# Kernel optimization log

Measured on AMD Instinct MI355X. Metric: run time of the kernel, lower is better.

Reference implementation:

```python
import jax, jax.numpy as jnp
import numpy as np

B, L, C, S, D = 2, 64, 256, 256, 512

def setup_inputs() -> dict:
    key = jax.random.key(0)
    ks = jax.random.split(key, 6)
    scale = 1.0 / np.sqrt(D)
    return {
        "queries": jax.random.normal(ks[0], (B, L, C, D), dtype=jnp.float32),
        "keys": jax.random.normal(ks[1], (B, L, S, D), dtype=jnp.float32),
        "values": jax.random.normal(ks[2], (B, L, S, D), dtype=jnp.float32),
        "Wq": jax.random.normal(ks[3], (D, D), dtype=jnp.float32) * scale,
        "bq": jnp.zeros((D,), dtype=jnp.float32),
        "Wkv": jax.random.normal(ks[4], (D, D), dtype=jnp.float32) * scale,
        "bkv": jnp.zeros((D,), dtype=jnp.float32),
        "Wo": jax.random.normal(ks[5], (D, D), dtype=jnp.float32) * scale,
        "bo": jnp.zeros((D,), dtype=jnp.float32),
    }

def reference(queries, keys, values, Wq, bq, Wkv, bkv, Wo, bo):
    d = queries.shape[-1]
    scale = 1.0 / jnp.sqrt(jnp.asarray(d, queries.dtype))
    # linear projections (torch Linear: x @ W.T + b); kv_projection shared for K and V
    q = queries @ Wq.T + bq            # [B, L, C, D]
    k = keys @ Wkv.T + bkv             # [B, L, S, D]
    v = values @ Wkv.T + bkv           # [B, L, S, D]
    scores = jnp.einsum('blcd,blsd->blcs', q, k)
    attn = jax.nn.softmax(scale * scores, axis=-1)  # dropout is identity in eval
    out = jnp.einsum('blcs,blsd->blcd', attn, v)
    return out @ Wo.T + bo
```

## Files before the change

kernel.cpp:

```cpp
#include <hip/hip_runtime.h>
#include <hip/hip_fp16.h>
#include <stdint.h>


typedef _Float16 f16;
typedef __attribute__((ext_vector_type(8))) _Float16 f16x8;
typedef __attribute__((ext_vector_type(4))) _Float16 f16x4;
typedef __attribute__((ext_vector_type(4))) float f32x4;

#define BK 64

__device__ __forceinline__ void glds16(const void* g, void* l)
{
    __builtin_amdgcn_global_load_lds(
        (const __attribute__((address_space(1))) void*)(uintptr_t)g,
        (__attribute__((address_space(3))) void*)(uint32_t)(uintptr_t)l,
        16, 0, 0);
}

__global__ __launch_bounds__(256)
void proj3(const float* __restrict__ qin, const float* __restrict__ kin,
           const float* __restrict__ vin, const f16* __restrict__ wq,
           const f16* __restrict__ wkv, const float* __restrict__ bq,
           const float* __restrict__ bkv, f16* __restrict__ qh,
           f16* __restrict__ kh, f16* __restrict__ vT)
{
    __shared__ __align__(16) float Asf[128][64];
    __shared__ __align__(16) f16  Bs[128][64];

    const int p     = blockIdx.x;
    const int which = p >> 10;
    const int inner = p & 1023;
    const int xcd   = inner & 7;
    const int slot  = inner >> 3;
    const int m0 = (xcd + 8 * (slot >> 2)) * 128;
    const int n0 = (slot & 3) * 128;

    const float* A    = (which == 0) ? qin : (which == 1) ? kin : vin;
    const f16*   Bt   = (which == 0) ? wq : wkv;
    const float* bias = (which == 0) ? bq : bkv;

    const int tid  = threadIdx.x;
    const int lane = tid & 63;
    const int wave = tid >> 6;
    const int quad = lane >> 4;
    const int l16  = lane & 15;
    const int wr   = wave >> 1;
    const int wc   = wave & 1;

    f32x4 acc[4][4];
    #pragma unroll
    for (int i = 0; i < 4; ++i)
        #pragma unroll
        for (int j = 0; j < 4; ++j)
            acc[i][j] = (f32x4){0.f, 0.f, 0.f, 0.f};

    const int i8 = lane >> 3;
    const int cl = (((lane & 7) - i8) & 7) * 8;

    const int ar4 = lane >> 4;

    for (int k0 = 0; k0 < 512; k0 += BK) {
        if (k0) __syncthreads();
        #pragma unroll
        for (int g = 0; g < 8; ++g) {
            const int R0  = (wave * 8 + g) * 4;
            const int row = R0 + ar4;
            const int gcol = ((lane & 15) - (row & 7)) & 15;
            glds16(A + (long)(m0 + row) * 512 + k0 + gcol * 4, &Asf[R0][0]);
        }
        #pragma unroll
        for (int g = 0; g < 4; ++g) {
            const int R0 = (wave * 4 + g) * 8;
            glds16(Bt + (long)(n0 + R0 + i8) * 512 + k0 + cl, &Bs[R0][0]);
        }
        __syncthreads();

        #pragma unroll
        for (int ksub = 0; ksub < 2; ++ksub) {
            f16x8 af[4], bf[4];
            #pragma unroll
            for (int i = 0; i < 4; ++i) {
                const int r  = wr * 64 + i * 16 + l16;
                const int g0 = ksub * 8 + quad * 2;
                const int ga = (g0 + (r & 7)) & 15;
                const int gb = (g0 + 1 + (r & 7)) & 15;
                const f32x4 a0 = *(const f32x4*)&Asf[r][ga * 4];
                const f32x4 a1 = *(const f32x4*)&Asf[r][gb * 4];
                f16x8 v;
                v[0] = (f16)a0[0]; v[1] = (f16)a0[1];
                v[2] = (f16)a0[2]; v[3] = (f16)a0[3];
                v[4] = (f16)a1[0]; v[5] = (f16)a1[1];
                v[6] = (f16)a1[2]; v[7] = (f16)a1[3];
                af[i] = v;
            }
            #pragma unroll
            for (int j = 0; j < 4; ++j) {
                const int r  = wc * 64 + j * 16 + l16;
                const int pc = ((ksub * 32 + quad * 8) + ((r & 7) * 8)) & 63;
                bf[j] = *(const f16x8*)&Bs[r][pc];
            }
            #pragma unroll
            for (int i = 0; i < 4; ++i)
                #pragma unroll
                for (int j = 0; j < 4; ++j)
                    acc[i][j] = __builtin_amdgcn_mfma_f32_16x16x32_f16(
                        af[i], bf[j], acc[i][j], 0, 0, 0);
        }
    }

    f16* qout = (which == 0) ? qh : kh;
    #pragma unroll
    for (int i = 0; i < 4; ++i) {
        #pragma unroll
        for (int j = 0; j < 4; ++j) {
            const int col = n0 + wc * 64 + j * 16 + l16;
            const float bv = bias[col];
            #pragma unroll
            for (int r = 0; r < 4; ++r) {
                const int row = m0 + wr * 64 + i * 16 + quad * 4 + r;
                const float val = acc[i][j][r] + bv;
                if (which == 2)
                    vT[(long)(row >> 8) * 131072 + (long)col * 256 + (row & 255)] = (f16)val;
                else
                    qout[(long)row * 512 + col] = (f16)val;
            }
        }
    }
}

__global__ __launch_bounds__(256)
void gemm_out(const f16* __restrict__ Ah, const f16* __restrict__ Bt,
              const float* __restrict__ bias, float* __restrict__ C)
{
    __shared__ f16 As[128][64];
    __shared__ f16 Bs[128][64];

    const int p    = blockIdx.x;
    const int xcd  = p & 7;
    const int slot = p >> 3;
    const int m0 = (xcd + 8 * (slot >> 2)) * 128;
    const int n0 = (slot & 3) * 128;

    const int tid  = threadIdx.x;
    const int lane = tid & 63;
    const int wave = tid >> 6;
    const int quad = lane >> 4;
    const int l16  = lane & 15;
    const int wr   = wave >> 1;
    const int wc   = wave & 1;

    f32x4 acc[4][4];
    #pragma unroll
    for (int i = 0; i < 4; ++i)
        #pragma unroll
        for (int j = 0; j < 4; ++j)
            acc[i][j] = (f32x4){0.f, 0.f, 0.f, 0.f};

    const int i8 = lane >> 3;
    const int cl = (((lane & 7) - i8) & 7) * 8;

    for (int k0 = 0; k0 < 512; k0 += BK) {
        if (k0) __syncthreads();
        #pragma unroll
        for (int j = 0; j < 4; ++j) {
            const int R0 = (wave * 4 + j) * 8;
            glds16(Ah + (long)(m0 + R0 + i8) * 512 + k0 + cl, &As[R0][0]);
            glds16(Bt + (long)(n0 + R0 + i8) * 512 + k0 + cl, &Bs[R0][0]);
        }
        __syncthreads();

        #pragma unroll
        for (int ksub = 0; ksub < 2; ++ksub) {
            f16x8 af[4], bf[4];
            #pragma unroll
            for (int i = 0; i < 4; ++i) {
                const int r  = wr * 64 + i * 16 + l16;
                const int pc = ((ksub * 32 + quad * 8) + ((r & 7) * 8)) & 63;
                af[i] = *(const f16x8*)&As[r][pc];
            }
            #pragma unroll
            for (int j = 0; j < 4; ++j) {
                const int r  = wc * 64 + j * 16 + l16;
                const int pc = ((ksub * 32 + quad * 8) + ((r & 7) * 8)) & 63;
                bf[j] = *(const f16x8*)&Bs[r][pc];
            }
            #pragma unroll
            for (int i = 0; i < 4; ++i)
                #pragma unroll
                for (int j = 0; j < 4; ++j)
                    acc[i][j] = __builtin_amdgcn_mfma_f32_16x16x32_f16(
                        af[i], bf[j], acc[i][j], 0, 0, 0);
        }
    }

    #pragma unroll
    for (int i = 0; i < 4; ++i) {
        #pragma unroll
        for (int j = 0; j < 4; ++j) {
            const int col = n0 + wc * 64 + j * 16 + l16;
            const float bv = bias[col];
            #pragma unroll
            for (int r = 0; r < 4; ++r) {
                const int row = m0 + wr * 64 + i * 16 + quad * 4 + r;
                C[(long)row * 512 + col] = acc[i][j][r] + bv;
            }
        }
    }
}

__global__ __launch_bounds__(512)
void attn_fused(const f16* __restrict__ q, const f16* __restrict__ k,
                const f16* __restrict__ vT, f16* __restrict__ O)
{
    __shared__ __align__(16) f16 bufA[128 * 256];
    __shared__ __align__(16) f16 Vs[4][128][64];
    __shared__ float red[2][128][4];

    f16 (*As)[BK]  = (f16(*)[BK])bufA;
    f16 (*Bs)[BK]  = (f16(*)[BK])(bufA + 128 * 64);
    f16 (*Ps)[256] = (f16(*)[256])bufA;

    const int p    = blockIdx.x;
    const int xcd  = p & 7;
    const int slot = p >> 3;
    const int z    = xcd + 8 * (slot >> 1);
    const int m0   = (slot & 1) * 128;

    const int tid  = threadIdx.x;
    const int lane = tid & 63;
    const int wave = tid >> 6;
    const int quad = lane >> 4;
    const int l16  = lane & 15;
    const int wr   = wave >> 2;
    const int wc   = wave & 3;

    const f16* Aq = q  + (long)z * 131072 + (long)m0 * 512;
    const f16* Bk = k  + (long)z * 131072;
    const f16* Vt = vT + (long)z * 131072;

    f32x4 acc[4][4];
    #pragma unroll
    for (int i = 0; i < 4; ++i)
        #pragma unroll
        for (int j = 0; j < 4; ++j)
            acc[i][j] = (f32x4){0.f, 0.f, 0.f, 0.f};

    const int i8 = lane >> 3;
    const int cl = (((lane & 7) - i8) & 7) * 8;

    for (int k0 = 0; k0 < 512; k0 += BK) {
        if (k0) __syncthreads();
        #pragma unroll
        for (int g = 0; g < 2; ++g) {
            const int R0 = (wave * 2 + g) * 8;
            glds16(Aq + (long)(R0 + i8) * 512 + k0 + cl, &As[R0][0]);
        }
        #pragma unroll
        for (int g = 0; g < 4; ++g) {
            const int R0 = (wave * 4 + g) * 8;
            glds16(Bk + (long)(R0 + i8) * 512 + k0 + cl, &Bs[R0][0]);
        }
        __syncthreads();

        #pragma unroll
        for (int ksub = 0; ksub < 2; ++ksub) {
            f16x8 af[4], bf[4];
            #pragma unroll
            for (int i = 0; i < 4; ++i) {
                const int r  = wr * 64 + i * 16 + l16;
                const int pc = ((ksub * 32 + quad * 8) + ((r & 7) * 8)) & 63;
                af[i] = *(const f16x8*)&As[r][pc];
            }
            #pragma unroll
            for (int j = 0; j < 4; ++j) {
                const int r  = wc * 64 + j * 16 + l16;
                const int pc = ((ksub * 32 + quad * 8) + ((r & 7) * 8)) & 63;
                bf[j] = *(const f16x8*)&Bs[r][pc];
            }
            #pragma unroll
            for (int i = 0; i < 4; ++i)
                #pragma unroll
                for (int j = 0; j < 4; ++j)
                    acc[i][j] = __builtin_amdgcn_mfma_f32_16x16x32_f16(
                        af[i], bf[j], acc[i][j], 0, 0, 0);
        }
    }

    const float scale = 0.044194173824159216f;
    float st[4][4];
    #pragma unroll
    for (int i = 0; i < 4; ++i)
        #pragma unroll
        for (int r = 0; r < 4; ++r) {
            float m = acc[i][0][r];
            #pragma unroll
            for (int j = 1; j < 4; ++j) m = fmaxf(m, acc[i][j][r]);
            st[i][r] = m;
        }
    #pragma unroll
    for (int off = 1; off < 16; off <<= 1)
        #pragma unroll
        for (int i = 0; i < 4; ++i)
            #pragma unroll
            for (int r = 0; r < 4; ++r)
                st[i][r] = fmaxf(st[i][r], __shfl_xor(st[i][r], off, 64));
    if (l16 == 0)
        #pragma unroll
        for (int i = 0; i < 4; ++i)
            #pragma unroll
            for (int r = 0; r < 4; ++r)
                red[0][wr * 64 + i * 16 + quad * 4 + r][wc] = st[i][r];
    __syncthreads();

    #pragma unroll
    for (int i = 0; i < 4; ++i)
        #pragma unroll
        for (int r = 0; r < 4; ++r) {
            const int row = wr * 64 + i * 16 + quad * 4 + r;
            const float m = fmaxf(fmaxf(red[0][row][0], red[0][row][1]),
                                  fmaxf(red[0][row][2], red[0][row][3]));
            float s = 0.f;
            #pragma unroll
            for (int j = 0; j < 4; ++j) {
                const float e = __expf(scale * (acc[i][j][r] - m));
                s += e;
                const int col = wc * 64 + j * 16 + l16;
                Ps[row][(col & 192) + (((col & 63) + ((row & 7) * 8)) & 63)] = (f16)e;
            }
            st[i][r] = s;
        }
    #pragma unroll
    for (int off = 1; off < 16; off <<= 1)
        #pragma unroll
        for (int i = 0; i < 4; ++i)
            #pragma unroll
            for (int r = 0; r < 4; ++r)
                st[i][r] += __shfl_xor(st[i][r], off, 64);
    if (l16 == 0)
        #pragma unroll
        for (int i = 0; i < 4; ++i)
            #pragma unroll
            for (int r = 0; r < 4; ++r)
                red[1][wr * 64 + i * 16 + quad * 4 + r][wc] = st[i][r];
    __syncthreads();

    if (tid < 128) {
        const float s = red[1][tid][0] + red[1][tid][1] +
                        red[1][tid][2] + red[1][tid][3];
        red[0][tid][0] = 1.0f / s;
    }

    for (int nc = 0; nc < 4; ++nc) {
        const int n0c = nc * 128;
        __syncthreads();
        #pragma unroll
        for (int kb = 0; kb < 4; ++kb)
            #pragma unroll
            for (int g = 0; g < 2; ++g) {
                const int R0 = (wave * 2 + g) * 8;
                glds16(Vt + (long)(n0c + R0 + i8) * 256 + kb * 64 + cl,
                       &Vs[kb][R0][0]);
            }
        __syncthreads();

        f32x4 acc2[4][2];
        #pragma unroll
        for (int i = 0; i < 4; ++i)
            #pragma unroll
            for (int j = 0; j < 2; ++j)
                acc2[i][j] = (f32x4){0.f, 0.f, 0.f, 0.f};

        #pragma unroll
        for (int kb = 0; kb < 4; ++kb)
            #pragma unroll
            for (int ksub = 0; ksub < 2; ++ksub) {
                f16x8 af[4], bf[2];
                #pragma unroll
                for (int i = 0; i < 4; ++i) {
                    const int r  = wr * 64 + i * 16 + l16;
                    const int pc = kb * 64 +
                        (((ksub * 32 + quad * 8) + ((r & 7) * 8)) & 63);
                    af[i] = *(const f16x8*)&Ps[r][pc];
                }
                #pragma unroll
                for (int j = 0; j < 2; ++j) {
                    const int rv = wc * 32 + j * 16 + l16;
                    const int pc = ((ksub * 32 + quad * 8) + ((rv & 7) * 8)) & 63;
                    bf[j] = *(const f16x8*)&Vs[kb][rv][pc];
                }
                #pragma unroll
                for (int i = 0; i < 4; ++i)
                    #pragma unroll
                    for (int j = 0; j < 2; ++j)
                        acc2[i][j] = __builtin_amdgcn_mfma_f32_16x16x32_f16(
                            af[i], bf[j], acc2[i][j], 0, 0, 0);
            }

        #pragma unroll
        for (int i = 0; i < 4; ++i)
            #pragma unroll
            for (int j = 0; j < 2; ++j) {
                const int col = n0c + wc * 32 + j * 16 + l16;
                #pragma unroll
                for (int rr = 0; rr < 4; ++rr) {
                    const int row = wr * 64 + i * 16 + quad * 4 + rr;
                    const float inv = red[0][row][0];
                    O[(long)z * 131072 + (long)(m0 + row) * 512 + col] =
                        (f16)(acc2[i][j][rr] * inv);
                }
            }
    }
}

__global__ __launch_bounds__(256)
void cvt3(const float* __restrict__ a, const float* __restrict__ b,
          const float* __restrict__ c, f16* __restrict__ oa,
          f16* __restrict__ ob, f16* __restrict__ oc)
{
    const int w = blockIdx.x >> 8;
    const int t = ((blockIdx.x & 255) * 256 + threadIdx.x) * 4;
    const float* src = (w == 0) ? a : (w == 1) ? b : c;
    f16* dst = (w == 0) ? oa : (w == 1) ? ob : oc;
    const float4 v = *(const float4*)(src + t);
    f16x4 o;
    o[0] = (f16)v.x; o[1] = (f16)v.y; o[2] = (f16)v.z; o[3] = (f16)v.w;
    *(f16x4*)(dst + t) = o;
}

extern "C" void kernel_launch(void* const* d_in, const int* in_sizes, int n_in,
                              void* d_out, int out_size, void* d_ws, size_t ws_size,
                              hipStream_t stream)
{
    const float* queries = (const float*)d_in[0];
    const float* keys    = (const float*)d_in[1];
    const float* values  = (const float*)d_in[2];
    const float* Wq      = (const float*)d_in[3];
    const float* bq      = (const float*)d_in[4];
    const float* Wkv     = (const float*)d_in[5];
    const float* bkv     = (const float*)d_in[6];
    const float* Wo      = (const float*)d_in[7];
    const float* bo      = (const float*)d_in[8];
    float* out = (float*)d_out;

    f16* ws  = (f16*)d_ws;
    f16* wq  = ws;
    f16* wkv = ws + 262144;
    f16* wo  = ws + 524288;
    f16* qh  = ws + 786432;
    f16* kh  = qh + 16777216;
    f16* vT  = kh + 16777216;
    f16* ao  = qh;

    cvt3<<<768, 256, 0, stream>>>(Wq, Wkv, Wo, wq, wkv, wo);

    proj3<<<3072, dim3(256), 0, stream>>>(
        queries, keys, values, wq, wkv, bq, bkv, qh, kh, vT);

    attn_fused<<<256, 512, 0, stream>>>(qh, kh, vT, ao);

    gemm_out<<<1024, dim3(256), 0, stream>>>(ao, wo, bo, out);
}
```

Measured before the change: 360.0 us.

## Double-buffer LDS tiles in projection, output, and attention kernels

Converts the K-loops of the projection GEMM, output GEMM, QK^T stage and PV stage to double-buffered LDS staging, so the next tile's global_load_lds is issued before computing on the current one. This is meant to overlap global memory latency with MFMA work and cut one barrier per iteration. GEMMs shrink their K step from 64 to 32 with new swizzles, and attention reorganizes shared memory into one buffer. In exchange there are more loop iterations and barriers, and a risk that async LDS loads are not complete at the barrier.

```diff
diff --git a/kernel.cpp b/kernel.cpp
--- a/kernel.cpp
+++ b/kernel.cpp
@@ -7,8 +7,6 @@
 typedef __attribute__((ext_vector_type(8))) _Float16 f16x8;
 typedef __attribute__((ext_vector_type(4))) _Float16 f16x4;
 typedef __attribute__((ext_vector_type(4))) float f32x4;
-
-#define BK 64
 
 __device__ __forceinline__ void glds16(const void* g, void* l)
 {
@@ -25,8 +23,8 @@
            const float* __restrict__ bkv, f16* __restrict__ qh,
            f16* __restrict__ kh, f16* __restrict__ vT)
 {
-    __shared__ __align__(16) float Asf[128][64];
-    __shared__ __align__(16) f16  Bs[128][64];
+    __shared__ __align__(16) float Asf[2][128][32];
+    __shared__ __align__(16) f16  Bs[2][128][32];
 
     const int p     = blockIdx.x;
     const int which = p >> 10;
@@ -55,58 +53,61 @@
         for (int j = 0; j < 4; ++j)
             acc[i][j] = (f32x4){0.f, 0.f, 0.f, 0.f};
 
-    const int i8 = lane >> 3;
-    const int cl = (((lane & 7) - i8) & 7) * 8;
-
-    const int ar4 = lane >> 4;
-
-    for (int k0 = 0; k0 < 512; k0 += BK) {
-        if (k0) __syncthreads();
-        #pragma unroll
-        for (int g = 0; g < 8; ++g) {
-            const int R0  = (wave * 8 + g) * 4;
-            const int row = R0 + ar4;
-            const int gcol = ((lane & 15) - (row & 7)) & 15;
-            glds16(A + (long)(m0 + row) * 512 + k0 + gcol * 4, &Asf[R0][0]);
-        }
+    const int arow = lane >> 3;
+    const int ags  = ((lane & 7) - arow) & 7;
+    const int brow = lane >> 2;
+    const int bgs  = ((lane & 3) - (brow & 3)) & 3;
+
+    auto stage = [&](int b, int k0) {
         #pragma unroll
         for (int g = 0; g < 4; ++g) {
             const int R0 = (wave * 4 + g) * 8;
-            glds16(Bt + (long)(n0 + R0 + i8) * 512 + k0 + cl, &Bs[R0][0]);
-        }
-        __syncthreads();
-
-        #pragma unroll
-        for (int ksub = 0; ksub < 2; ++ksub) {
-            f16x8 af[4], bf[4];
-            #pragma unroll
-            for (int i = 0; i < 4; ++i) {
-                const int r  = wr * 64 + i * 16 + l16;
-                const int g0 = ksub * 8 + quad * 2;
-                const int ga = (g0 + (r & 7)) & 15;
-                const int gb = (g0 + 1 + (r & 7)) & 15;
-                const f32x4 a0 = *(const f32x4*)&Asf[r][ga * 4];
-                const f32x4 a1 = *(const f32x4*)&Asf[r][gb * 4];
-                f16x8 v;
-                v[0] = (f16)a0[0]; v[1] = (f16)a0[1];
-                v[2] = (f16)a0[2]; v[3] = (f16)a0[3];
-                v[4] = (f16)a1[0]; v[5] = (f16)a1[1];
-                v[6] = (f16)a1[2]; v[7] = (f16)a1[3];
-                af[i] = v;
-            }
-            #pragma unroll
-            for (int j = 0; j < 4; ++j) {
-                const int r  = wc * 64 + j * 16 + l16;
-                const int pc = ((ksub * 32 + quad * 8) + ((r & 7) * 8)) & 63;
-                bf[j] = *(const f16x8*)&Bs[r][pc];
-            }
-            #pragma unroll
-            for (int i = 0; i < 4; ++i)
-                #pragma unroll
-                for (int j = 0; j < 4; ++j)
-                    acc[i][j] = __builtin_amdgcn_mfma_f32_16x16x32_f16(
-                        af[i], bf[j], acc[i][j], 0, 0, 0);
-        }
+            glds16(A + (long)(m0 + R0 + arow) * 512 + k0 + ags * 4,
+                   &Asf[b][R0][0]);
+        }
+        #pragma unroll
+        for (int g = 0; g < 2; ++g) {
+            const int R0 = (wave * 2 + g) * 16;
+            glds16(Bt + (long)(n0 + R0 + brow) * 512 + k0 + bgs * 8,
+                   &Bs[b][R0][0]);
+        }
+    };
+
+    stage(0, 0);
+    __syncthreads();
+    for (int t = 0; t < 16; ++t) {
+        const int b = t & 1;
+        if (t < 15) stage(b ^ 1, (t + 1) * 32);
+
+        f16x8 af[4], bf[4];
+        #pragma unroll
+        for (int i = 0; i < 4; ++i) {
+            const int r  = wr * 64 + i * 16 + l16;
+            const int ga = (quad * 2 + (r & 7)) & 7;
+            const int gb = (quad * 2 + 1 + (r & 7)) & 7;
+            const f32x4 a0 = *(const f32x4*)&Asf[b][r][ga * 4];
+            const f32x4 a1 = *(const f32x4*)&Asf[b][r][gb * 4];
+            f16x8 v;
+            v[0] = (f16)a0[0]; v[1] = (f16)a0[1];
+            v[2] = (f16)a0[2]; v[3] = (f16)a0[3];
+            v[4] = (f16)a1[0]; v[5] = (f16)a1[1];
+            v[6] = (f16)a1[2]; v[7] = (f16)a1[3];
+            af[i] = v;
+        }
+        #pragma unroll
+        for (int j = 0; j < 4; ++j) {
+            const int r  = wc * 64 + j * 16 + l16;
+            const int gp = (quad + (r & 3)) & 3;
+            bf[j] = *(const f16x8*)&Bs[b][r][gp * 8];
+        }
+        #pragma unroll
+        for (int i = 0; i < 4; ++i)
+            #pragma unroll
+            for (int j = 0; j < 4; ++j)
+                acc[i][j] = __builtin_amdgcn_mfma_f32_16x16x32_f16(
+                    af[i], bf[j], acc[i][j], 0, 0, 0);
+
+        if (t < 15) __syncthreads();
     }
 
     f16* qout = (which == 0) ? qh : kh;
@@ -133,8 +134,8 @@
 void gemm_out(const f16* __restrict__ Ah, const f16* __restrict__ Bt,
               const float* __restrict__ bias, float* __restrict__ C)
 {
-    __shared__ f16 As[128][64];
-    __shared__ f16 Bs[128][64];
+    __shared__ __align__(16) f16 As[2][128][32];
+    __shared__ __align__(16) f16 Bs[2][128][32];
 
     const int p    = blockIdx.x;
     const int xcd  = p & 7;
@@ -157,41 +158,47 @@
         for (int j = 0; j < 4; ++j)
             acc[i][j] = (f32x4){0.f, 0.f, 0.f, 0.f};
 
-    const int i8 = lane >> 3;
-    const int cl = (((lane & 7) - i8) & 7) * 8;
-
-    for (int k0 = 0; k0 < 512; k0 += BK) {
-        if (k0) __syncthreads();
+    const int brow = lane >> 2;
+    const int bgs  = ((lane & 3) - (brow & 3)) & 3;
+
+    auto stage = [&](int b, int k0) {
+        #pragma unroll
+        for (int g = 0; g < 2; ++g) {
+            const int R0 = (wave * 2 + g) * 16;
+            glds16(Ah + (long)(m0 + R0 + brow) * 512 + k0 + bgs * 8,
+                   &As[b][R0][0]);
+            glds16(Bt + (long)(n0 + R0 + brow) * 512 + k0 + bgs * 8,
+                   &Bs[b][R0][0]);
+        }
+    };
+
+    stage(0, 0);
+    __syncthreads();
+    for (int t = 0; t < 16; ++t) {
+        const int b = t & 1;
+        if (t < 15) stage(b ^ 1, (t + 1) * 32);
+
+        f16x8 af[4], bf[4];
+        #pragma unroll
+        for (int i = 0; i < 4; ++i) {
+            const int r  = wr * 64 + i * 16 + l16;
+            const int ga = (quad + (r & 3)) & 3;
+            af[i] = *(const f16x8*)&As[b][r][ga * 8];
+        }
         #pragma unroll
         for (int j = 0; j < 4; ++j) {
-            const int R0 = (wave * 4 + j) * 8;
-            glds16(Ah + (long)(m0 + R0 + i8) * 512 + k0 + cl, &As[R0][0]);
-            glds16(Bt + (long)(n0 + R0 + i8) * 512 + k0 + cl, &Bs[R0][0]);
-        }
-        __syncthreads();
-
-        #pragma unroll
-        for (int ksub = 0; ksub < 2; ++ksub) {
-            f16x8 af[4], bf[4];
-            #pragma unroll
-            for (int i = 0; i < 4; ++i) {
-                const int r  = wr * 64 + i * 16 + l16;
-                const int pc = ((ksub * 32 + quad * 8) + ((r & 7) * 8)) & 63;
-                af[i] = *(const f16x8*)&As[r][pc];
-            }
-            #pragma unroll
-            for (int j = 0; j < 4; ++j) {
-                const int r  = wc * 64 + j * 16 + l16;
-                const int pc = ((ksub * 32 + quad * 8) + ((r & 7) * 8)) & 63;
-                bf[j] = *(const f16x8*)&Bs[r][pc];
-            }
-            #pragma unroll
-            for (int i = 0; i < 4; ++i)
-                #pragma unroll
-                for (int j = 0; j < 4; ++j)
-                    acc[i][j] = __builtin_amdgcn_mfma_f32_16x16x32_f16(
-                        af[i], bf[j], acc[i][j], 0, 0, 0);
-        }
+            const int r  = wc * 64 + j * 16 + l16;
+            const int gb = (quad + (r & 3)) & 3;
+            bf[j] = *(const f16x8*)&Bs[b][r][gb * 8];
+        }
+        #pragma unroll
+        for (int i = 0; i < 4; ++i)
+            #pragma unroll
+            for (int j = 0; j < 4; ++j)
+                acc[i][j] = __builtin_amdgcn_mfma_f32_16x16x32_f16(
+                    af[i], bf[j], acc[i][j], 0, 0, 0);
+
+        if (t < 15) __syncthreads();
     }
 
     #pragma unroll
@@ -213,13 +220,13 @@
 void attn_fused(const f16* __restrict__ q, const f16* __restrict__ k,
                 const f16* __restrict__ vT, f16* __restrict__ O)
 {
-    __shared__ __align__(16) f16 bufA[128 * 256];
-    __shared__ __align__(16) f16 Vs[4][128][64];
+    __shared__ __align__(16) f16 big[49152];
     __shared__ float red[2][128][4];
 
-    f16 (*As)[BK]  = (f16(*)[BK])bufA;
-    f16 (*Bs)[BK]  = (f16(*)[BK])(bufA + 128 * 64);
-    f16 (*Ps)[256] = (f16(*)[256])bufA;
+    f16 (*As2)[128][64] = (f16(*)[128][64])big;
+    f16 (*Bs2)[256][64] = (f16(*)[256][64])(big + 16384);
+    f16 (*Ps)[256]      = (f16(*)[256])big;
+    f16 (*Vs2)[128][64] = (f16(*)[128][64])(big + 32768);
 
     const int p    = blockIdx.x;
     const int xcd  = p & 7;
@@ -249,19 +256,24 @@
     const int i8 = lane >> 3;
     const int cl = (((lane & 7) - i8) & 7) * 8;
 
-    for (int k0 = 0; k0 < 512; k0 += BK) {
-        if (k0) __syncthreads();
+    auto stage1 = [&](int b, int k0) {
         #pragma unroll
         for (int g = 0; g < 2; ++g) {
             const int R0 = (wave * 2 + g) * 8;
-            glds16(Aq + (long)(R0 + i8) * 512 + k0 + cl, &As[R0][0]);
+            glds16(Aq + (long)(R0 + i8) * 512 + k0 + cl, &As2[b][R0][0]);
         }
         #pragma unroll
         for (int g = 0; g < 4; ++g) {
             const int R0 = (wave * 4 + g) * 8;
-            glds16(Bk + (long)(R0 + i8) * 512 + k0 + cl, &Bs[R0][0]);
-        }
-        __syncthreads();
+            glds16(Bk + (long)(R0 + i8) * 512 + k0 + cl, &Bs2[b][R0][0]);
+        }
+    };
+
+    stage1(0, 0);
+    __syncthreads();
+    for (int ks = 0; ks < 8; ++ks) {
+        const int b = ks & 1;
+        if (ks < 7) stage1(b ^ 1, (ks + 1) * 64);
 
         #pragma unroll
         for (int ksub = 0; ksub < 2; ++ksub) {
@@ -270,13 +282,13 @@
             for (int i = 0; i < 4; ++i) {
                 const int r  = wr * 64 + i * 16 + l16;
                 const int pc = ((ksub * 32 + quad * 8) + ((r & 7) * 8)) & 63;
-                af[i] = *(const f16x8*)&As[r][pc];
+                af[i] = *(const f16x8*)&As2[b][r][pc];
             }
             #pragma unroll
             for (int j = 0; j < 4; ++j) {
                 const int r  = wc * 64 + j * 16 + l16;
                 const int pc = ((ksub * 32 + quad * 8) + ((r & 7) * 8)) & 63;
-                bf[j] = *(const f16x8*)&Bs[r][pc];
+                bf[j] = *(const f16x8*)&Bs2[b][r][pc];
             }
             #pragma unroll
             for (int i = 0; i < 4; ++i)
@@ -285,6 +297,7 @@
                     acc[i][j] = __builtin_amdgcn_mfma_f32_16x16x32_f16(
                         af[i], bf[j], acc[i][j], 0, 0, 0);
         }
+        if (ks < 7) __syncthreads();
     }
 
     const float scale = 0.044194173824159216f;
@@ -351,65 +364,74 @@
         red[0][tid][0] = 1.0f / s;
     }
 
-    for (int nc = 0; nc < 4; ++nc) {
-        const int n0c = nc * 128;
-        __syncthreads();
-        #pragma unroll
-        for (int kb = 0; kb < 4; ++kb)
-            #pragma unroll
-            for (int g = 0; g < 2; ++g) {
-                const int R0 = (wave * 2 + g) * 8;
-                glds16(Vt + (long)(n0c + R0 + i8) * 256 + kb * 64 + cl,
-                       &Vs[kb][R0][0]);
-            }
-        __syncthreads();
-
-        f32x4 acc2[4][2];
-        #pragma unroll
-        for (int i = 0; i < 4; ++i)
-            #pragma unroll
-            for (int j = 0; j < 2; ++j)
-                acc2[i][j] = (f32x4){0.f, 0.f, 0.f, 0.f};
-
-        #pragma unroll
-        for (int kb = 0; kb < 4; ++kb)
-            #pragma unroll
-            for (int ksub = 0; ksub < 2; ++ksub) {
-                f16x8 af[4], bf[2];
+    auto stageV = [&](int b, int it) {
+        const int nc = it >> 2, kb = it & 3;
+        #pragma unroll
+        for (int g = 0; g < 2; ++g) {
+            const int R0 = (wave * 2 + g) * 8;
+            glds16(Vt + (long)(nc * 128 + R0 + i8) * 256 + kb * 64 + cl,
+                   &Vs2[b][R0][0]);
+        }
+    };
+
+    stageV(0, 0);
+    __syncthreads();
+
+    f32x4 acc2[4][2];
+    for (int it = 0; it < 16; ++it) {
+        const int b  = it & 1;
+        const int nc = it >> 2;
+        const int kb = it & 3;
+        if (it < 15) stageV(b ^ 1, it + 1);
+
+        if (kb == 0) {
+            #pragma unroll
+            for (int i = 0; i < 4; ++i)
                 #pragma unroll
-                for (int i = 0; i < 4; ++i) {
-                    const int r  = wr * 64 + i * 16 + l16;
-                    const int pc = kb * 64 +
-                        (((ksub * 32 + quad * 8) + ((r & 7) * 8)) & 63);
-                    af[i] = *(const f16x8*)&Ps[r][pc];
-                }
+                for (int j = 0; j < 2; ++j)
+                    acc2[i][j] = (f32x4){0.f, 0.f, 0.f, 0.f};
+        }
+
+        #pragma unroll
+        for (int ksub = 0; ksub < 2; ++ksub) {
+            f16x8 af[4], bf[2];
+            #pragma unroll
+            for (int i = 0; i < 4; ++i) {
+                const int r  = wr * 64 + i * 16 + l16;
+                const int pc = kb * 64 +
+                    (((ksub * 32 + quad * 8) + ((r & 7) * 8)) & 63);
+                af[i] = *(const f16x8*)&Ps[r][pc];
+            }
+            #pragma unroll
+            for (int j = 0; j < 2; ++j) {
+                const int rv = wc * 32 + j * 16 + l16;
+                const int pc = ((ksub * 32 + quad * 8) + ((rv & 7) * 8)) & 63;
+                bf[j] = *(const f16x8*)&Vs2[b][rv][pc];
+            }
+            #pragma unroll
+            for (int i = 0; i < 4; ++i)
+                #pragma unroll
+                for (int j = 0; j < 2; ++j)
+                    acc2[i][j] = __builtin_amdgcn_mfma_f32_16x16x32_f16(
+                        af[i], bf[j], acc2[i][j], 0, 0, 0);
+        }
+
+        if (kb == 3) {
+            #pragma unroll
+            for (int i = 0; i < 4; ++i)
                 #pragma unroll
                 for (int j = 0; j < 2; ++j) {
-                    const int rv = wc * 32 + j * 16 + l16;
-                    const int pc = ((ksub * 32 + quad * 8) + ((rv & 7) * 8)) & 63;
-                    bf[j] = *(const f16x8*)&Vs[kb][rv][pc];
+                    const int col = nc * 128 + wc * 32 + j * 16 + l16;
+                    #pragma unroll
+                    for (int rr = 0; rr < 4; ++rr) {
+                        const int row = wr * 64 + i * 16 + quad * 4 + rr;
+                        const float inv = red[0][row][0];
+                        O[(long)z * 131072 + (long)(m0 + row) * 512 + col] =
+                            (f16)(acc2[i][j][rr] * inv);
+                    }
                 }
-                #pragma unroll
-                for (int i = 0; i < 4; ++i)
-                    #pragma unroll
-                    for (int j = 0; j < 2; ++j)
-                        acc2[i][j] = __builtin_amdgcn_mfma_f32_16x16x32_f16(
-                            af[i], bf[j], acc2[i][j], 0, 0, 0);
-            }
-
-        #pragma unroll
-        for (int i = 0; i < 4; ++i)
-            #pragma unroll
-            for (int j = 0; j < 2; ++j) {
-                const int col = n0c + wc * 32 + j * 16 + l16;
-                #pragma unroll
-                for (int rr = 0; rr < 4; ++rr) {
-                    const int row = wr * 64 + i * 16 + quad * 4 + rr;
-                    const float inv = red[0][row][0];
-                    O[(long)z * 131072 + (long)(m0 + row) * 512 + col] =
-                        (f16)(acc2[i][j][rr] * inv);
-                }
-            }
+        }
+        if (it < 15) __syncthreads();
     }
 }
 
```

After: 368.5 us. +2.4%, slower.
